# Kernel tuning notes

Hardware: AMD Instinct MI355X
Metric: run time of the kernel (lower is better)

Reference implementation:

```python
import jax, jax.numpy as jnp
import numpy as np

EPS = 1e-7  # tf.keras.backend.epsilon()
NUM_HEADS = 8


def setup_inputs() -> dict:
    key = jax.random.key(0)
    ks = jax.random.split(key, 7)
    B, H, W, C = 4, 128, 128, 512
    glorot = (2.0 / (C + C)) ** 0.5
    x = jax.random.normal(ks[0], (B, H, W, C), dtype=jnp.float32)
    wq = jax.random.normal(ks[1], (C, C), dtype=jnp.float32) * glorot
    bq = jnp.zeros((C,), dtype=jnp.float32)
    wk = jax.random.normal(ks[2], (C, C), dtype=jnp.float32) * glorot
    bk = jnp.zeros((C,), dtype=jnp.float32)
    wv = jax.random.normal(ks[3], (C, C), dtype=jnp.float32) * glorot
    bv = jnp.zeros((C,), dtype=jnp.float32)
    return {"x": x, "wq": wq, "bq": bq, "wk": wk, "bk": bk, "wv": wv, "bv": bv}


def _axial_attention(query, key, value, num_heads):
    B, H, W, C = value.shape
    d = query.shape[-1] // num_heads
    q5 = query.reshape(B, H, W, num_heads, d)
    k5 = key.reshape(B, H, W, num_heads, d)
    # column (vertical) attention: scores over H, per column w -> [B, nh, W, H, H]
    v_att = jnp.einsum("bhwnd,bgwnd->bnwhg", q5, k5)
    # row (horizontal) attention: scores over W, per row h -> [B, nh, H, W, W]
    u_att = jnp.einsum("bhwnd,bhvnd->bnhwv", q5, k5)
    # faithful clip-before-softmax chain from the original module
    v_att = jnp.clip(v_att, -1.0 + EPS, 1.0 - EPS)
    u_att = jnp.clip(u_att, -1.0 + EPS, 1.0 - EPS)
    scale = jnp.sqrt(jnp.asarray(d, dtype=v_att.dtype))
    v_att = v_att / scale
    u_att = u_att / scale
    # safed_softmax: softmax in fp32 (inputs already fp32 here)
    v_att = jax.nn.softmax(v_att.astype(jnp.float32), axis=-1).astype(query.dtype)
    u_att = jax.nn.softmax(u_att.astype(jnp.float32), axis=-1).astype(query.dtype)
    v_att = jnp.where(jnp.isnan(v_att), EPS, v_att)
    u_att = jnp.where(jnp.isnan(u_att), EPS, u_att)
    v_att = jnp.clip(v_att, EPS, 1.0 - EPS)
    u_att = jnp.clip(u_att, EPS, 1.0 - EPS)
    # value: [B, nh, W, H, d]
    val5 = value.reshape(B, H, W, num_heads, d)
    xv = jnp.einsum("bnwhg,bnwgd->bnhwd", v_att, val5.transpose(0, 3, 2, 1, 4))
    xu = jnp.einsum("bnhwv,bnhvd->bnhwd", u_att, xv)
    # transpose (0,2,3,4,1): head index becomes last -> channels ordered [d, nh]
    out = xu.transpose(0, 2, 3, 4, 1).reshape(B, H, W, d * num_heads)
    return out


def reference(x, wq, bq, wk, bk, wv, bv):
    # 1x1 convs == per-pixel dense projections
    query = jnp.einsum("bhwc,cf->bhwf", x, wq) + bq
    key = jnp.einsum("bhwc,cf->bhwf", x, wk) + bk
    value = jnp.einsum("bhwc,cf->bhwf", x, wv) + bv
    return _axial_attention(query, key, value, NUM_HEADS)
```

## Files before the change

### kernel.cpp

```cpp
#include <hip/hip_runtime.h>

typedef unsigned short ush;
typedef __attribute__((ext_vector_type(8))) __bf16 bf16x8;
typedef __attribute__((ext_vector_type(4))) float f32x4;

#define NE 33554432L

__device__ __forceinline__ float b2f(ush u) {
  return __uint_as_float(((unsigned int)u) << 16);
}
__device__ __forceinline__ ush f2b(float f) {
  unsigned int x = __float_as_uint(f);
  x += 0x7fffu + ((x >> 16) & 1u);
  return (ush)(x >> 16);
}
__device__ __forceinline__ bf16x8 bc8(int4 v) { return __builtin_bit_cast(bf16x8, v); }

__device__ __forceinline__ void gload16(const ush* g, ush* l) {
  __builtin_amdgcn_global_load_lds(
      (const __attribute__((address_space(1))) void*)g,
      (__attribute__((address_space(3))) void*)l, 16, 0, 0);
}

__global__ __launch_bounds__(256)
void detect_dtype(const ush* __restrict__ x, int* __restrict__ flag) {
  __shared__ int red[256];
  const int t = threadIdx.x;
  int cnt = 0;
  for (int i = t; i < 16384; i += 256) {
    const int e = (x[i] >> 7) & 0xFF;
    cnt += (e == 0 || (e >= 100 && e <= 142)) ? 1 : 0;
  }
  red[t] = cnt;
  __syncthreads();
  for (int s = 128; s > 0; s >>= 1) {
    if (t < s) red[t] += red[t + s];
    __syncthreads();
  }
  if (t == 0) flag[0] = (red[0] >= 13107) ? 1 : 0;
}

__global__ __launch_bounds__(256)
void pack_x(const void* __restrict__ xin, ush* __restrict__ xb,
            const int* __restrict__ flag) {
  const long i0 = ((long)blockIdx.x * 256 + threadIdx.x) * 8;
  if (*flag) {
    *(int4*)&xb[i0] = *(const int4*)&((const ush*)xin)[i0];
  } else {
    const float* xf = (const float*)xin;
    const float4 a = *(const float4*)&xf[i0];
    const float4 b = *(const float4*)&xf[i0 + 4];
    union { ush u[8]; int4 v; } r;
    r.u[0] = f2b(a.x); r.u[1] = f2b(a.y); r.u[2] = f2b(a.z); r.u[3] = f2b(a.w);
    r.u[4] = f2b(b.x); r.u[5] = f2b(b.y); r.u[6] = f2b(b.z); r.u[7] = f2b(b.w);
    *(int4*)&xb[i0] = r.v;
  }
}

__global__ __launch_bounds__(256)
void pack_w(const void* __restrict__ w0, const void* __restrict__ w1,
            const void* __restrict__ w2, ush* __restrict__ wTb,
            const int* __restrict__ flag) {
  __shared__ ush tile[32][33];
  const void* w = (blockIdx.z == 0) ? w0 : ((blockIdx.z == 1) ? w1 : w2);
  ush* wT = wTb + (long)blockIdx.z * 262144;
  const int bx = blockIdx.x * 32, by = blockIdx.y * 32;
  const int tx = threadIdx.x & 31, ty = threadIdx.x >> 5;
  const int f = *flag;
#pragma unroll
  for (int j = 0; j < 32; j += 8) {
    const int k = by + ty + j, n = bx + tx;
    tile[ty + j][tx] = f ? ((const ush*)w)[k * 512 + n]
                         : f2b(((const float*)w)[k * 512 + n]);
  }
  __syncthreads();
#pragma unroll
  for (int j = 0; j < 32; j += 8)
    wT[(bx + ty + j) * 512 + by + tx] = tile[tx][ty + j];
}

__global__ void pack_bias(const void* __restrict__ b0, const void* __restrict__ b1,
                          const void* __restrict__ b2, float* __restrict__ biasf,
                          const int* __restrict__ flag) {
  const void* b = (blockIdx.x == 0) ? b0 : ((blockIdx.x == 1) ? b1 : b2);
  const int n = threadIdx.x;
  const float v = (*flag) ? b2f(((const ush*)b)[n]) : ((const float*)b)[n];
  biasf[blockIdx.x * 512 + n] = v;
}

__global__ __launch_bounds__(256)
void proj_gemm(const ush* __restrict__ xb, const ush* __restrict__ wTb,
               const float* __restrict__ biasf, ush* __restrict__ qkv) {
  __shared__ ush As[2][4096];
  __shared__ ush Bs[2][4096];

  const int lin = blockIdx.x + (blockIdx.y << 2) + (blockIdx.z << 11);
  const int swz = ((lin & 7) * 768) + (lin >> 3);
  const int z   = swz >> 11;
  const int rem = swz & 2047;
  const int by  = rem >> 2, bx = rem & 3;

  const ush* wt = wTb + (long)z * 262144;
  const float* bias = biasf + z * 512;
  ush* out = qkv + (long)z * NE;

  const int t = threadIdx.x;
  const int lane = t & 63;
  const int wvid = t >> 6;
  const int wm = wvid & 1, wn = wvid >> 1;
  const int col = lane & 15, quad = lane >> 4;

  const long m0 = (long)by * 128;
  const int n0 = bx * 128;

  const int r_in_g = lane >> 2;
  const int swzk = (((lane & 3) ^ ((r_in_g >> 1) & 3)) * 8);
  const int g0 = wvid * 2, g1 = g0 + 1;
  const ush* gA0 = xb + (m0 + g0 * 16 + r_in_g) * 512 + swzk;
  const ush* gA1 = xb + (m0 + g1 * 16 + r_in_g) * 512 + swzk;
  const ush* gB0 = wt + (long)(n0 + g0 * 16 + r_in_g) * 512 + swzk;
  const ush* gB1 = wt + (long)(n0 + g1 * 16 + r_in_g) * 512 + swzk;

  const int kswz = ((quad ^ ((col >> 1) & 3)) * 8);
  int aofs[4], bofs4[4];
#pragma unroll
  for (int i = 0; i < 4; i++) aofs[i] = (wm * 64 + i * 16 + col) * 32 + kswz;
#pragma unroll
  for (int j = 0; j < 4; j++) bofs4[j] = (wn * 64 + j * 16 + col) * 32 + kswz;

  const f32x4 z4 = {0.f, 0.f, 0.f, 0.f};
  f32x4 acc[4][4];
#pragma unroll
  for (int i = 0; i < 4; i++)
#pragma unroll
    for (int j = 0; j < 4; j++) acc[i][j] = z4;

  gload16(gA0, &As[0][g0 * 512]);
  gload16(gA1, &As[0][g1 * 512]);
  gload16(gB0, &Bs[0][g0 * 512]);
  gload16(gB1, &Bs[0][g1 * 512]);
  __syncthreads();

  int cur = 0;
  for (int k0 = 0; k0 < 512; k0 += 32) {
    const int nk = k0 + 32;
    if (nk < 512) {
      const int nb = cur ^ 1;
      gload16(gA0 + nk, &As[nb][g0 * 512]);
      gload16(gA1 + nk, &As[nb][g1 * 512]);
      gload16(gB0 + nk, &Bs[nb][g0 * 512]);
      gload16(gB1 + nk, &Bs[nb][g1 * 512]);
    }
    bf16x8 a[4], b[4];
#pragma unroll
    for (int i = 0; i < 4; i++) a[i] = bc8(*(const int4*)&As[cur][aofs[i]]);
#pragma unroll
    for (int j = 0; j < 4; j++) b[j] = bc8(*(const int4*)&Bs[cur][bofs4[j]]);
#pragma unroll
    for (int i = 0; i < 4; i++)
#pragma unroll
      for (int j = 0; j < 4; j++)
        acc[i][j] = __builtin_amdgcn_mfma_f32_16x16x32_bf16(a[i], b[j], acc[i][j], 0, 0, 0);
    __syncthreads();
    cur ^= 1;
  }

#pragma unroll
  for (int j = 0; j < 4; j++) {
    const int n = n0 + wn * 64 + j * 16 + col;
    const float bb = bias[n];
#pragma unroll
    for (int i = 0; i < 4; i++) {
      const long row0 = m0 + wm * 64 + i * 16 + quad * 4;
#pragma unroll
      for (int r = 0; r < 4; r++)
        out[(row0 + r) * 512 + n] = f2b(acc[i][j][r] + bb);
    }
  }
}

#define QS_STRIDE 72
#define VT_STRIDE 136
#define P_STRIDE  136
#define OS_STRIDE 72

__device__ __forceinline__ int vt_idx(int d, int g) {
  return d * VT_STRIDE + ((((g >> 3) ^ ((d >> 3) & 7)) << 3) | (g & 7));
}

template<int PASS>
__global__ __launch_bounds__(512, 4)
void axial_attn_mfma(const ush* __restrict__ Qb, const ush* __restrict__ Kb,
                     ush* __restrict__ Vb, float* __restrict__ xuf,
                     const int bofs) {
  __shared__ ush smem[(PASS == 1) ? 36352 : 27136];
  ush* Qs = smem;
  ush* Ks = smem + 9216;
  ush* Vt = smem + 18432;
  ush* P  = smem;
  ush* Os = smem + 27136;

  const int pp = blockIdx.x;
  const int NH = (PASS == 1) ? 8 : 4;
  const int b = blockIdx.y + ((PASS == 1) ? 0 : bofs);
  const int nstart = (PASS == 1) ? 0 : (blockIdx.z * 4);

  long base0; int stride;
  if (PASS == 1) { base0 = ((long)b * 16384 + pp) * 512; stride = 65536; }
  else           { base0 = ((long)(b * 128 + pp) * 128) * 512; stride = 512; }

  const int t = threadIdx.x;
  const int srow0 = t >> 3, c8 = t & 7;
  const long o0 = base0 + (long)srow0 * stride + c8 * 8;
  const long o1 = base0 + (long)(srow0 + 64) * stride + c8 * 8;

  const int lane = t & 63, wv = t >> 6;
  const int col = lane & 15, quad = lane >> 4;
  const int m0 = wv * 16;
  const f32x4 z4 = {0.f, 0.f, 0.f, 0.f};
  const float CLIP = 1.0f - 1e-7f;

  int4 qr0, qr1, kr0, kr1, vr0, vr1;
#define LOADH(nn_) do { const long nn = (long)(nn_) * 64;          \
    qr0 = *(const int4*)(Qb + o0 + nn); qr1 = *(const int4*)(Qb + o1 + nn); \
    kr0 = *(const int4*)(Kb + o0 + nn); kr1 = *(const int4*)(Kb + o1 + nn); \
    vr0 = *(const int4*)(Vb + o0 + nn); vr1 = *(const int4*)(Vb + o1 + nn); \
  } while (0)

  LOADH(nstart);

  for (int hn = 0; hn < NH; ++hn) {
    const int n = nstart + hn;
    *(int4*)&Qs[srow0 * QS_STRIDE + c8 * 8] = qr0;
    *(int4*)&Qs[(srow0 + 64) * QS_STRIDE + c8 * 8] = qr1;
    *(int4*)&Ks[srow0 * QS_STRIDE + c8 * 8] = kr0;
    *(int4*)&Ks[(srow0 + 64) * QS_STRIDE + c8 * 8] = kr1;
    {
      union { int4 i4; ush u[8]; } vu;
      vu.i4 = vr0;
#pragma unroll
      for (int dd = 0; dd < 8; dd++) Vt[vt_idx(c8 * 8 + dd, srow0)] = vu.u[dd];
      vu.i4 = vr1;
#pragma unroll
      for (int dd = 0; dd < 8; dd++) Vt[vt_idx(c8 * 8 + dd, srow0 + 64)] = vu.u[dd];
    }
    __syncthreads();
    if (hn + 1 < NH) LOADH(n + 1);

    f32x4 sacc[8];
#pragma unroll
    for (int j = 0; j < 8; j++) sacc[j] = z4;
    __builtin_amdgcn_s_setprio(1);
#pragma unroll
    for (int k0 = 0; k0 < 64; k0 += 32) {
      bf16x8 a, kb[8];
      a = bc8(*(const int4*)&Qs[(m0 + col) * QS_STRIDE + k0 + quad * 8]);
#pragma unroll
      for (int j = 0; j < 8; j++)
        kb[j] = bc8(*(const int4*)&Ks[(j * 16 + col) * QS_STRIDE + k0 + quad * 8]);
#pragma unroll
      for (int j = 0; j < 8; j++)
        sacc[j] = __builtin_amdgcn_mfma_f32_16x16x32_bf16(a, kb[j], sacc[j], 0, 0, 0);
    }
    __builtin_amdgcn_s_setprio(0);

    float e[8][4], inv[4];
#pragma unroll
    for (int r = 0; r < 4; r++) {
      float part = 0.f;
#pragma unroll
      for (int j = 0; j < 8; j++) {
        float s = sacc[j][r];
        s = fminf(fmaxf(s, -CLIP), CLIP) * 0.125f;
        const float ee = __expf(s);
        e[j][r] = ee;
        part += ee;
      }
      part += __shfl_xor(part, 1);
      part += __shfl_xor(part, 2);
      part += __shfl_xor(part, 4);
      part += __shfl_xor(part, 8);
      inv[r] = 1.0f / part;
    }
    __syncthreads();

#pragma unroll
    for (int r = 0; r < 4; r++) {
      const int row = m0 + quad * 4 + r;
#pragma unroll
      for (int j = 0; j < 8; j++) {
        const float pv = fminf(fmaxf(e[j][r] * inv[r], 1e-7f), CLIP);
        P[row * P_STRIDE + j * 16 + col] = f2b(pv);
      }
    }
    __syncthreads();

    f32x4 oacc[4];
#pragma unroll
    for (int j = 0; j < 4; j++) oacc[j] = z4;
    __builtin_amdgcn_s_setprio(1);
#pragma unroll
    for (int k0 = 0; k0 < 128; k0 += 32) {
      bf16x8 a, vb[4];
      a = bc8(*(const int4*)&P[(m0 + col) * P_STRIDE + k0 + quad * 8]);
#pragma unroll
      for (int j = 0; j < 4; j++)
        vb[j] = bc8(*(const int4*)&Vt[vt_idx(j * 16 + col, k0 + quad * 8)]);
#pragma unroll
      for (int j = 0; j < 4; j++)
        oacc[j] = __builtin_amdgcn_mfma_f32_16x16x32_bf16(a, vb[j], oacc[j], 0, 0, 0);
    }
    __builtin_amdgcn_s_setprio(0);
    __syncthreads();

    if (PASS == 1) {
#pragma unroll
      for (int r = 0; r < 4; r++) {
        const int row = m0 + quad * 4 + r;
#pragma unroll
        for (int j = 0; j < 4; j++)
          Os[row * OS_STRIDE + j * 16 + col] = f2b(oacc[j][r]);
      }
      __syncthreads();
      *(int4*)&Vb[o0 + (long)n * 64] = *(const int4*)&Os[srow0 * OS_STRIDE + c8 * 8];
      *(int4*)&Vb[o1 + (long)n * 64] = *(const int4*)&Os[(srow0 + 64) * OS_STRIDE + c8 * 8];
    } else {
      const long xbase = (((long)(blockIdx.y * 8 + n) * 128 + pp) * 128) * 64;
#pragma unroll
      for (int r = 0; r < 4; r++) {
        const int row = m0 + quad * 4 + r;
#pragma unroll
        for (int j = 0; j < 4; j++)
          xuf[xbase + (long)row * 64 + j * 16 + col] = oacc[j][r];
      }
    }
  }
#undef LOADH
}

__global__ __launch_bounds__(256)
void out_interleave(const float* __restrict__ xu, void* __restrict__ outp,
                    const int* __restrict__ flagp, const int bofs) {
  __shared__ float lds[8192];
  const int bz = blockIdx.z, h = blockIdx.y, w0 = blockIdx.x * 16;
  const int t = threadIdx.x;
#pragma unroll
  for (int n = 0; n < 8; n++) {
    const float* src = xu + ((((long)(bz * 8 + n)) * 128 + h) * 128 + w0) * 64;
    const int e = t * 4, w = e >> 6, d = e & 63;
    const float4 v = *(const float4*)&src[e];
    const int dr = (d + n * 8) & 63;
    *(float4*)&lds[(n * 16 + w) * 64 + dr] = v;
  }
  __syncthreads();
  const int flg = *flagp;
  const long obase = (((long)(bz + bofs) * 128 + h) * 128 + w0) * 512;
  const int tc = t & 127, c0 = tc * 4;
  const int d = c0 >> 3, n0 = c0 & 7;
#pragma unroll
  for (int ro = 0; ro < 8; ro++) {
    const int w = (t >> 7) * 8 + ro;
    float r[4];
#pragma unroll
    for (int k = 0; k < 4; k++) {
      const int n = n0 + k;
      r[k] = lds[(n * 16 + w) * 64 + ((d + n * 8) & 63)];
    }
    const long oi = obase + (long)w * 512 + c0;
    if (flg) {
      union { ush u[4]; int2 v; } o;
      o.u[0] = f2b(r[0]); o.u[1] = f2b(r[1]);
      o.u[2] = f2b(r[2]); o.u[3] = f2b(r[3]);
      *(int2*)&((ush*)outp)[oi] = o.v;
    } else {
      float4 o; o.x = r[0]; o.y = r[1]; o.z = r[2]; o.w = r[3];
      *(float4*)&((float*)outp)[oi] = o;
    }
  }
}

extern "C" void kernel_launch(void* const* d_in, const int* in_sizes, int n_in,
                              void* d_out, int out_size, void* d_ws, size_t ws_size,
                              hipStream_t stream) {
  const void* x  = d_in[0];
  const void* wq = d_in[1];
  const void* bq = d_in[2];
  const void* wk = d_in[3];
  const void* bk = d_in[4];
  const void* wv = d_in[5];
  const void* bv = d_in[6];

  char* ws = (char*)d_ws;
  int*   flag  = (int*)ws;
  float* biasf = (float*)(ws + 256);
  ush*   wTb   = (ush*)(ws + 8192);
  ush*   xb    = (ush*)(ws + 8192 + 1572864);
  float* xuf   = (float*)(ws + 8192 + 1572864);
  ush*   qkv   = (ush*)(ws + 8192 + 1572864 + 67108864);

  dim3 blk(256);
  detect_dtype<<<1, blk, 0, stream>>>((const ush*)x, flag);
  pack_bias<<<3, 512, 0, stream>>>(bq, bk, bv, biasf, flag);
  pack_w<<<dim3(16, 16, 3), blk, 0, stream>>>(wq, wk, wv, wTb, flag);
  pack_x<<<16384, blk, 0, stream>>>(x, xb, flag);

  ush* Q = qkv;
  ush* K = Q + NE;
  ush* V = K + NE;
  proj_gemm<<<dim3(4, 512, 3), blk, 0, stream>>>(xb, wTb, biasf, Q);
  axial_attn_mfma<1><<<dim3(128, 4), dim3(512), 0, stream>>>(Q, K, V, nullptr, 0);
  for (int half = 0; half < 2; half++) {
    axial_attn_mfma<2><<<dim3(128, 2, 2), dim3(512), 0, stream>>>(Q, K, V, xuf, half * 2);
    out_interleave<<<dim3(8, 128, 2), blk, 0, stream>>>(xuf, d_out, flag, half * 2);
  }
}
```

Baseline: 550.4 us.

## Enlarge projection GEMM tiles with triple-buffered LDS pipeline; bf16 xu staging path

The projection GEMM moves from 128x128 tiles with 256 threads and double buffering to 256x256 tiles with 512 threads, a 3-stage global_load_lds pipeline using explicit vmcnt waits and raw barriers, an XCD-aware block remap, and MFMA priority boosting. The aim is more data reuse per LDS load and better overlap of global loads with MFMA work. Separately, when inputs are bf16, the pass-2 attention kernel writes its xu intermediate as bf16 rather than fp32, and out_interleave reads it back as bf16, which halves that intermediate traffic. The costs are higher register pressure from the 8x4 accumulator tile and an extra bf16 rounding of the intermediate in the bf16 path.

```diff
diff --git a/kernel.cpp b/kernel.cpp
--- a/kernel.cpp
+++ b/kernel.cpp
@@ -88,93 +88,100 @@
   biasf[blockIdx.x * 512 + n] = v;
 }
 
-__global__ __launch_bounds__(256)
+__global__ __launch_bounds__(512, 2)
 void proj_gemm(const ush* __restrict__ xb, const ush* __restrict__ wTb,
                const float* __restrict__ biasf, ush* __restrict__ qkv) {
-  __shared__ ush As[2][4096];
-  __shared__ ush Bs[2][4096];
-
-  const int lin = blockIdx.x + (blockIdx.y << 2) + (blockIdx.z << 11);
-  const int swz = ((lin & 7) * 768) + (lin >> 3);
-  const int z   = swz >> 11;
-  const int rem = swz & 2047;
-  const int by  = rem >> 2, bx = rem & 3;
+  __shared__ ush plds[49152];
+
+  const int lin = blockIdx.x;
+  const int wg = (lin & 7) * 192 + (lin >> 3);
+  const int mb = wg & 255, nb = (wg >> 8) & 1, z = wg >> 9;
 
   const ush* wt = wTb + (long)z * 262144;
   const float* bias = biasf + z * 512;
   ush* out = qkv + (long)z * NE;
 
   const int t = threadIdx.x;
-  const int lane = t & 63;
-  const int wvid = t >> 6;
-  const int wm = wvid & 1, wn = wvid >> 1;
+  const int lane = t & 63, wvid = t >> 6;
+  const int wm = wvid >> 2, wn = wvid & 3;
   const int col = lane & 15, quad = lane >> 4;
 
-  const long m0 = (long)by * 128;
-  const int n0 = bx * 128;
-
-  const int r_in_g = lane >> 2;
-  const int swzk = (((lane & 3) ^ ((r_in_g >> 1) & 3)) * 8);
-  const int g0 = wvid * 2, g1 = g0 + 1;
-  const ush* gA0 = xb + (m0 + g0 * 16 + r_in_g) * 512 + swzk;
-  const ush* gA1 = xb + (m0 + g1 * 16 + r_in_g) * 512 + swzk;
-  const ush* gB0 = wt + (long)(n0 + g0 * 16 + r_in_g) * 512 + swzk;
-  const ush* gB1 = wt + (long)(n0 + g1 * 16 + r_in_g) * 512 + swzk;
-
-  const int kswz = ((quad ^ ((col >> 1) & 3)) * 8);
-  int aofs[4], bofs4[4];
-#pragma unroll
-  for (int i = 0; i < 4; i++) aofs[i] = (wm * 64 + i * 16 + col) * 32 + kswz;
-#pragma unroll
-  for (int j = 0; j < 4; j++) bofs4[j] = (wn * 64 + j * 16 + col) * 32 + kswz;
+  const long m0 = (long)mb * 256;
+  const int n0 = nb * 256;
+
+  const int srow = lane >> 2;
+  const int sslot = ((lane & 3) ^ ((lane >> 3) & 3)) * 8;
+  const ush* gA0 = xb + (m0 + wvid * 16 + srow) * 512 + sslot;
+  const ush* gA1 = xb + (m0 + 128 + wvid * 16 + srow) * 512 + sslot;
+  const ush* gB0 = wt + (long)(n0 + wvid * 16 + srow) * 512 + sslot;
+  const ush* gB1 = wt + (long)(n0 + 128 + wvid * 16 + srow) * 512 + sslot;
+  const int dA0 = wvid * 512;
+  const int dA1 = 4096 + wvid * 512;
+
+  const int kofs = ((quad ^ ((col >> 1) & 3)) * 8);
+
+#define PSTAGE(buf, kt) do {                              \
+    ush* ab_ = plds + (buf) * 16384;                      \
+    const int ko_ = (kt) * 32;                            \
+    gload16(gA0 + ko_, ab_ + dA0);                        \
+    gload16(gA1 + ko_, ab_ + dA1);                        \
+    gload16(gB0 + ko_, ab_ + 8192 + dA0);                 \
+    gload16(gB1 + ko_, ab_ + 8192 + dA1);                 \
+  } while (0)
 
   const f32x4 z4 = {0.f, 0.f, 0.f, 0.f};
-  f32x4 acc[4][4];
-#pragma unroll
-  for (int i = 0; i < 4; i++)
-#pragma unroll
-    for (int j = 0; j < 4; j++) acc[i][j] = z4;
-
-  gload16(gA0, &As[0][g0 * 512]);
-  gload16(gA1, &As[0][g1 * 512]);
-  gload16(gB0, &Bs[0][g0 * 512]);
-  gload16(gB1, &Bs[0][g1 * 512]);
-  __syncthreads();
+  f32x4 acc[8][4];
+#pragma unroll
+  for (int mt = 0; mt < 8; mt++)
+#pragma unroll
+    for (int nt = 0; nt < 4; nt++) acc[mt][nt] = z4;
+
+  PSTAGE(0, 0);
+  PSTAGE(1, 1);
+  asm volatile("s_waitcnt vmcnt(4)" ::: "memory");
+  asm volatile("s_barrier" ::: "memory");
 
   int cur = 0;
-  for (int k0 = 0; k0 < 512; k0 += 32) {
-    const int nk = k0 + 32;
-    if (nk < 512) {
-      const int nb = cur ^ 1;
-      gload16(gA0 + nk, &As[nb][g0 * 512]);
-      gload16(gA1 + nk, &As[nb][g1 * 512]);
-      gload16(gB0 + nk, &Bs[nb][g0 * 512]);
-      gload16(gB1 + nk, &Bs[nb][g1 * 512]);
-    }
-    bf16x8 a[4], b[4];
-#pragma unroll
-    for (int i = 0; i < 4; i++) a[i] = bc8(*(const int4*)&As[cur][aofs[i]]);
-#pragma unroll
-    for (int j = 0; j < 4; j++) b[j] = bc8(*(const int4*)&Bs[cur][bofs4[j]]);
-#pragma unroll
-    for (int i = 0; i < 4; i++)
-#pragma unroll
-      for (int j = 0; j < 4; j++)
-        acc[i][j] = __builtin_amdgcn_mfma_f32_16x16x32_bf16(a[i], b[j], acc[i][j], 0, 0, 0);
-    __syncthreads();
-    cur ^= 1;
-  }
-
-#pragma unroll
-  for (int j = 0; j < 4; j++) {
-    const int n = n0 + wn * 64 + j * 16 + col;
-    const float bb = bias[n];
-#pragma unroll
-    for (int i = 0; i < 4; i++) {
-      const long row0 = m0 + wm * 64 + i * 16 + quad * 4;
+  for (int kt = 0; kt < 16; ++kt) {
+    if (kt < 14) {
+      int n2 = cur + 2; if (n2 >= 3) n2 -= 3;
+      PSTAGE(n2, kt + 2);
+    }
+    const ush* Ab = plds + cur * 16384;
+    const ush* Bb = Ab + 8192;
+    bf16x8 a[8], bb[4];
+#pragma unroll
+    for (int mt = 0; mt < 8; mt++)
+      a[mt] = bc8(*(const int4*)&Ab[(wm * 128 + mt * 16 + col) * 32 + kofs]);
+#pragma unroll
+    for (int nt = 0; nt < 4; nt++)
+      bb[nt] = bc8(*(const int4*)&Bb[(wn * 64 + nt * 16 + col) * 32 + kofs]);
+    __builtin_amdgcn_s_setprio(1);
+#pragma unroll
+    for (int mt = 0; mt < 8; mt++)
+#pragma unroll
+      for (int nt = 0; nt < 4; nt++)
+        acc[mt][nt] = __builtin_amdgcn_mfma_f32_16x16x32_bf16(a[mt], bb[nt], acc[mt][nt], 0, 0, 0);
+    __builtin_amdgcn_s_setprio(0);
+    if (kt < 15) {
+      if (kt < 14) asm volatile("s_waitcnt vmcnt(4)" ::: "memory");
+      else         asm volatile("s_waitcnt vmcnt(0)" ::: "memory");
+      asm volatile("s_barrier" ::: "memory");
+    }
+    cur = (cur < 2) ? cur + 1 : 0;
+  }
+#undef PSTAGE
+
+#pragma unroll
+  for (int nt = 0; nt < 4; nt++) {
+    const int n = n0 + wn * 64 + nt * 16 + col;
+    const float bbv = bias[n];
+#pragma unroll
+    for (int mt = 0; mt < 8; mt++) {
+      const long row0 = m0 + wm * 128 + mt * 16 + quad * 4;
 #pragma unroll
       for (int r = 0; r < 4; r++)
-        out[(row0 + r) * 512 + n] = f2b(acc[i][j][r] + bb);
+        out[(row0 + r) * 512 + n] = f2b(acc[mt][nt][r] + bbv);
     }
   }
 }
@@ -191,8 +198,8 @@
 template<int PASS>
 __global__ __launch_bounds__(512, 4)
 void axial_attn_mfma(const ush* __restrict__ Qb, const ush* __restrict__ Kb,
-                     ush* __restrict__ Vb, float* __restrict__ xuf,
-                     const int bofs) {
+                     ush* __restrict__ Vb, void* __restrict__ xuf,
+                     const int* __restrict__ flagp, const int bofs) {
   __shared__ ush smem[(PASS == 1) ? 36352 : 27136];
   ush* Qs = smem;
   ush* Ks = smem + 9216;
@@ -200,6 +207,7 @@
   ush* P  = smem;
   ush* Os = smem + 27136;
 
+  const int flg = (PASS == 2) ? *flagp : 0;
   const int pp = blockIdx.x;
   const int NH = (PASS == 1) ? 8 : 4;
   const int b = blockIdx.y + ((PASS == 1) ? 0 : bofs);
@@ -326,12 +334,24 @@
       *(int4*)&Vb[o1 + (long)n * 64] = *(const int4*)&Os[(srow0 + 64) * OS_STRIDE + c8 * 8];
     } else {
       const long xbase = (((long)(blockIdx.y * 8 + n) * 128 + pp) * 128) * 64;
-#pragma unroll
-      for (int r = 0; r < 4; r++) {
-        const int row = m0 + quad * 4 + r;
-#pragma unroll
-        for (int j = 0; j < 4; j++)
-          xuf[xbase + (long)row * 64 + j * 16 + col] = oacc[j][r];
+      if (flg) {
+        ush* xw = (ush*)xuf;
+#pragma unroll
+        for (int r = 0; r < 4; r++) {
+          const int row = m0 + quad * 4 + r;
+#pragma unroll
+          for (int j = 0; j < 4; j++)
+            xw[xbase + (long)row * 64 + j * 16 + col] = f2b(oacc[j][r]);
+        }
+      } else {
+        float* xf = (float*)xuf;
+#pragma unroll
+        for (int r = 0; r < 4; r++) {
+          const int row = m0 + quad * 4 + r;
+#pragma unroll
+          for (int j = 0; j < 4; j++)
+            xf[xbase + (long)row * 64 + j * 16 + col] = oacc[j][r];
+        }
       }
     }
   }
@@ -339,42 +359,57 @@
 }
 
 __global__ __launch_bounds__(256)
-void out_interleave(const float* __restrict__ xu, void* __restrict__ outp,
+void out_interleave(const void* __restrict__ xu, void* __restrict__ outp,
                     const int* __restrict__ flagp, const int bofs) {
-  __shared__ float lds[8192];
+  __shared__ float ldsf[8192];
   const int bz = blockIdx.z, h = blockIdx.y, w0 = blockIdx.x * 16;
   const int t = threadIdx.x;
-#pragma unroll
-  for (int n = 0; n < 8; n++) {
-    const float* src = xu + ((((long)(bz * 8 + n)) * 128 + h) * 128 + w0) * 64;
-    const int e = t * 4, w = e >> 6, d = e & 63;
-    const float4 v = *(const float4*)&src[e];
-    const int dr = (d + n * 8) & 63;
-    *(float4*)&lds[(n * 16 + w) * 64 + dr] = v;
-  }
-  __syncthreads();
   const int flg = *flagp;
   const long obase = (((long)(bz + bofs) * 128 + h) * 128 + w0) * 512;
   const int tc = t & 127, c0 = tc * 4;
   const int d = c0 >> 3, n0 = c0 & 7;
-#pragma unroll
-  for (int ro = 0; ro < 8; ro++) {
-    const int w = (t >> 7) * 8 + ro;
-    float r[4];
-#pragma unroll
-    for (int k = 0; k < 4; k++) {
-      const int n = n0 + k;
-      r[k] = lds[(n * 16 + w) * 64 + ((d + n * 8) & 63)];
-    }
-    const long oi = obase + (long)w * 512 + c0;
-    if (flg) {
+
+  if (flg) {
+    ush* lds = (ush*)ldsf;
+#pragma unroll
+    for (int n = 0; n < 8; n++) {
+      const ush* src = (const ush*)xu + ((((long)(bz * 8 + n)) * 128 + h) * 128 + w0) * 64;
+      const int e = t * 4, w = e >> 6, dd = e & 63;
+      const int2 v = *(const int2*)&src[e];
+      const int dr = (dd + n * 8) & 63;
+      *(int2*)&lds[(n * 16 + w) * 64 + dr] = v;
+    }
+    __syncthreads();
+#pragma unroll
+    for (int ro = 0; ro < 8; ro++) {
+      const int w = (t >> 7) * 8 + ro;
       union { ush u[4]; int2 v; } o;
-      o.u[0] = f2b(r[0]); o.u[1] = f2b(r[1]);
-      o.u[2] = f2b(r[2]); o.u[3] = f2b(r[3]);
-      *(int2*)&((ush*)outp)[oi] = o.v;
-    } else {
-      float4 o; o.x = r[0]; o.y = r[1]; o.z = r[2]; o.w = r[3];
-      *(float4*)&((float*)outp)[oi] = o;
+#pragma unroll
+      for (int k = 0; k < 4; k++) {
+        const int n = n0 + k;
+        o.u[k] = lds[(n * 16 + w) * 64 + ((d + n * 8) & 63)];
+      }
+      *(int2*)&((ush*)outp)[obase + (long)w * 512 + c0] = o.v;
+    }
+  } else {
+#pragma unroll
+    for (int n = 0; n < 8; n++) {
+      const float* src = (const float*)xu + ((((long)(bz * 8 + n)) * 128 + h) * 128 + w0) * 64;
+      const int e = t * 4, w = e >> 6, dd = e & 63;
+      const float4 v = *(const float4*)&src[e];
+      const int dr = (dd + n * 8) & 63;
+      *(float4*)&ldsf[(n * 16 + w) * 64 + dr] = v;
+    }
+    __syncthreads();
+#pragma unroll
+    for (int ro = 0; ro < 8; ro++) {
+      const int w = (t >> 7) * 8 + ro;
+      float4 o;
+      o.x = ldsf[((n0 + 0) * 16 + w) * 64 + ((d + (n0 + 0) * 8) & 63)];
+      o.y = ldsf[((n0 + 1) * 16 + w) * 64 + ((d + (n0 + 1) * 8) & 63)];
+      o.z = ldsf[((n0 + 2) * 16 + w) * 64 + ((d + (n0 + 2) * 8) & 63)];
+      o.w = ldsf[((n0 + 3) * 16 + w) * 64 + ((d + (n0 + 3) * 8) & 63)];
+      *(float4*)&((float*)outp)[obase + (long)w * 512 + c0] = o;
     }
   }
 }
@@ -395,7 +430,7 @@
   float* biasf = (float*)(ws + 256);
   ush*   wTb   = (ush*)(ws + 8192);
   ush*   xb    = (ush*)(ws + 8192 + 1572864);
-  float* xuf   = (float*)(ws + 8192 + 1572864);
+  void*  xuf   = (void*)(ws + 8192 + 1572864);
   ush*   qkv   = (ush*)(ws + 8192 + 1572864 + 67108864);
 
   dim3 blk(256);
@@ -407,10 +442,10 @@
   ush* Q = qkv;
   ush* K = Q + NE;
   ush* V = K + NE;
-  proj_gemm<<<dim3(4, 512, 3), blk, 0, stream>>>(xb, wTb, biasf, Q);
-  axial_attn_mfma<1><<<dim3(128, 4), dim3(512), 0, stream>>>(Q, K, V, nullptr, 0);
+  proj_gemm<<<1536, dim3(512), 0, stream>>>(xb, wTb, biasf, Q);
+  axial_attn_mfma<1><<<dim3(128, 4), dim3(512), 0, stream>>>(Q, K, V, nullptr, flag, 0);
   for (int half = 0; half < 2; half++) {
-    axial_attn_mfma<2><<<dim3(128, 2, 2), dim3(512), 0, stream>>>(Q, K, V, xuf, half * 2);
+    axial_attn_mfma<2><<<dim3(128, 2, 2), dim3(512), 0, stream>>>(Q, K, V, xuf, flag, half * 2);
     out_interleave<<<dim3(8, 128, 2), blk, 0, stream>>>(xuf, d_out, flag, half * 2);
   }
 }
```

Measured after the change: 603.8 us. 1.1x slower.
